# Optimization experiments

Measured on AMD Instinct MI355X. Metric: run time of the kernel, lower is better.

Reference implementation:

```python
import jax, jax.numpy as jnp
import numpy as np

N, D_IN, D_H, D_OUT, E = 32768, 1024, 2048, 1024, 8

def setup_inputs() -> dict:
    key = jax.random.key(0)
    ks = jax.random.split(key, 8)
    s_in = 1.0 / np.sqrt(D_IN)
    s_h = 1.0 / np.sqrt(D_H)
    return {
        "x": jax.random.normal(ks[0], (N, D_IN), dtype=jnp.float32),
        "Wr": jax.random.normal(ks[1], (D_IN, E), dtype=jnp.float32) * s_in,
        "br": jnp.zeros((E,), dtype=jnp.float32),
        "W1": jax.random.normal(ks[2], (E, D_IN, D_H), dtype=jnp.float32) * s_in,
        "b1": jnp.zeros((E, D_H), dtype=jnp.float32),
        "W2": jax.random.normal(ks[3], (E, D_H, D_OUT), dtype=jnp.float32) * s_h,
        "b2": jnp.zeros((E, D_OUT), dtype=jnp.float32),
    }

def reference(x, Wr, br, W1, b1, W2, b2):
    # Supervised router: encoder is Identity, router is Linear + softmax.
    router_probs = jax.nn.softmax(x @ Wr + br, axis=-1)            # [N, E]
    router_probs_max = jnp.max(router_probs, axis=-1)              # [N]
    routes = jnp.argmax(router_probs, axis=-1)                     # [N] int
    counts = jnp.sum(jax.nn.one_hot(routes, E, dtype=x.dtype), axis=0)  # [E]

    # Top-1 dispatch: each token goes through exactly one expert MLP.
    # Small fixed loop over experts (E=8); mask-combine replaces gather/scatter.
    out = jnp.zeros((N, D_OUT), dtype=x.dtype)
    for e in range(E):
        h = jax.nn.relu(x @ W1[e] + b1[e])                         # [N, D_H]
        y = h @ W2[e] + b2[e]                                      # [N, D_OUT]
        out = out + jnp.where((routes == e)[:, None], y, jnp.zeros((), x.dtype))
    # Straight-through scaling: value 1 in fwd, routes grad through router prob.
    scale = router_probs_max / jax.lax.stop_gradient(router_probs_max)
    out = out * scale[:, None]
    return out, router_probs, counts
```

## Files before the change

### kernel.cpp

```cpp
#include <hip/hip_runtime.h>
#include <stdint.h>


#define NTOK   32768
#define DIN    1024
#define DH     2048
#define DOUT   1024
#define NEXP   8

typedef unsigned short u16;
typedef __bf16 bf16x8 __attribute__((ext_vector_type(8)));
typedef float  f32x4  __attribute__((ext_vector_type(4)));
typedef const __attribute__((address_space(1))) void gvoid_t;
typedef __attribute__((address_space(3))) void svoid_t;

__device__ __forceinline__ u16 f2bf(float f) {
  union { float f; uint32_t u; } v; v.f = f;
  return (u16)((v.u + 0x7FFFu + ((v.u >> 16) & 1u)) >> 16);
}

__global__ __launch_bounds__(256) void k_router(
    const float* __restrict__ x, const float* __restrict__ Wr,
    const float* __restrict__ br, float* __restrict__ probs,
    int* __restrict__ routes, u16* __restrict__ xb)
{
  __shared__ float wr_s[NEXP * DIN];
  int tid = threadIdx.x;
  for (int idx = tid; idx < DIN * NEXP / 4; idx += 256) {
    float4 v = ((const float4*)Wr)[idx];
    int k = idx >> 1, r = (idx & 1) * 4;
    wr_s[(r + 0) * DIN + k] = v.x;
    wr_s[(r + 1) * DIN + k] = v.y;
    wr_s[(r + 2) * DIN + k] = v.z;
    wr_s[(r + 3) * DIN + k] = v.w;
  }
  __syncthreads();
  int lane = tid & 63, wv = tid >> 6;
  int t = blockIdx.x * 4 + wv;
  const float* xr = x + (size_t)t * DIN;
  u16* xbrow = xb + (size_t)t * DIN;
  float acc[NEXP];
  #pragma unroll
  for (int e = 0; e < NEXP; ++e) acc[e] = 0.f;
  #pragma unroll
  for (int i = 0; i < 4; ++i) {
    int k = i * 256 + lane * 4;
    float4 xv = *(const float4*)(xr + k);
    ushort4 o;
    o.x = f2bf(xv.x); o.y = f2bf(xv.y); o.z = f2bf(xv.z); o.w = f2bf(xv.w);
    *(ushort4*)(xbrow + k) = o;
    #pragma unroll
    for (int e = 0; e < NEXP; ++e) {
      float4 w4 = *(const float4*)(wr_s + e * DIN + k);
      acc[e] += xv.x * w4.x + xv.y * w4.y + xv.z * w4.z + xv.w * w4.w;
    }
  }
  #pragma unroll
  for (int off = 32; off >= 1; off >>= 1) {
    #pragma unroll
    for (int e = 0; e < NEXP; ++e) acc[e] += __shfl_xor(acc[e], off, 64);
  }
  if (lane == 0) {
    float l[NEXP], m = -1e30f;
    #pragma unroll
    for (int e = 0; e < NEXP; ++e) { l[e] = acc[e] + br[e]; m = fmaxf(m, l[e]); }
    float p[NEXP], s = 0.f;
    #pragma unroll
    for (int e = 0; e < NEXP; ++e) { p[e] = expf(l[e] - m); s += p[e]; }
    float inv = 1.f / s;
    int am = 0; float best = l[0];
    #pragma unroll
    for (int e = 1; e < NEXP; ++e) if (l[e] > best) { best = l[e]; am = e; }
    #pragma unroll
    for (int e = 0; e < NEXP; ++e) probs[(size_t)t * NEXP + e] = p[e] * inv;
    routes[t] = am;
  }
}

__global__ __launch_bounds__(256) void k_count(
    const int* __restrict__ routes, int* __restrict__ aux)
{
  int t = blockIdx.x * 256 + threadIdx.x;
  int e = routes[t];
  int lane = threadIdx.x & 63;
  #pragma unroll
  for (int ee = 0; ee < NEXP; ++ee) {
    unsigned long long m = __ballot(e == ee);
    if (lane == 0 && m) atomicAdd(&aux[ee], (int)__popcll(m));
  }
}

__global__ __launch_bounds__(256) void k_prefix(int* __restrict__ aux, float* __restrict__ counts_out)
{
  __shared__ int s_off[NEXP], s_cnt[NEXP], s_tb[NEXP], s_nt;
  int tid = threadIdx.x;
  if (tid == 0) {
    int off = 0, tb = 0;
    for (int e = 0; e < NEXP; ++e) {
      int c = aux[e];
      counts_out[e] = (float)c;
      s_cnt[e] = c; s_off[e] = off; s_tb[e] = tb;
      aux[24 + e] = off;
      off += c; tb += (c + 127) >> 7;
    }
    s_nt = tb;
    aux[16] = tb;
  }
  __syncthreads();
  int nt = s_nt;
  for (int i = tid; i < nt; i += 256) {
    int e = 0;
    #pragma unroll
    for (int k = 1; k < NEXP; ++k) if (i >= s_tb[k]) e = k;
    int tt = i - s_tb[e];
    aux[128 + i] = e;
    aux[512 + i] = s_off[e] + tt * 128;
    aux[896 + i] = s_off[e] + s_cnt[e];
  }
}

__global__ __launch_bounds__(256) void k_assign(
    const int* __restrict__ routes, int* __restrict__ aux,
    int* __restrict__ pos_of_tok, int* __restrict__ tok_of_pos)
{
  int t = blockIdx.x * 256 + threadIdx.x;
  int e = routes[t];
  int lane = threadIdx.x & 63;
  int p = 0;
  #pragma unroll
  for (int ee = 0; ee < NEXP; ++ee) {
    unsigned long long m = __ballot(e == ee);
    int base = 0;
    if (lane == 0 && m) base = atomicAdd(&aux[8 + ee], (int)__popcll(m));
    base = __shfl(base, 0, 64);
    if (e == ee)
      p = aux[24 + ee] + base + (int)__popcll(m & ((1ull << lane) - 1ull));
  }
  pos_of_tok[t] = p;
  tok_of_pos[p] = t;
}

__global__ __launch_bounds__(256) void k_transpose(
    const float* __restrict__ W1, u16* __restrict__ W1t,
    const float* __restrict__ W2, u16* __restrict__ W2t)
{
  int z = blockIdx.z;
  const float* src; u16* dst; int K, Nn, e;
  if (z < NEXP) { src = W1; dst = W1t; K = DIN; Nn = DH;   e = z; }
  else          { src = W2; dst = W2t; K = DH;  Nn = DOUT; e = z - NEXP; }
  int k0 = blockIdx.x * 64, n0 = blockIdx.y * 64;
  if (k0 >= K || n0 >= Nn) return;
  __shared__ float tile[64][65];
  const float* s = src + ((size_t)e * K + k0) * Nn + n0;
  int r = threadIdx.x >> 6, c = threadIdx.x & 63;
  #pragma unroll
  for (int i = 0; i < 16; ++i)
    tile[r + i * 4][c] = s[(size_t)(r + i * 4) * Nn + c];
  __syncthreads();
  u16* d = dst + ((size_t)e * Nn + n0) * K + k0;
  #pragma unroll
  for (int i = 0; i < 16; ++i) {
    int nr = r + i * 4;
    d[(size_t)nr * K + c] = f2bf(tile[c][nr]);
  }
}

template<int MODE, int GATHER>
__global__ __launch_bounds__(256, 4) void k_gemm(
    const u16* __restrict__ A, const u16* __restrict__ Bt,
    const float* __restrict__ bias, u16* __restrict__ Hout,
    float* __restrict__ Yout, const int* __restrict__ tok_of_pos,
    const int* __restrict__ aux, int K, int Nn, int nbyl)
{
  int nwg = gridDim.x;
  int bid = blockIdx.x;
  int wg  = (bid & 7) * (nwg >> 3) + (bid >> 3);
  int by  = wg & ((1 << nbyl) - 1);
  int bx  = wg >> nbyl;
  if (bx >= aux[16]) return;
  int e  = aux[128 + bx];
  int r0 = aux[512 + bx];
  int r1 = aux[896 + bx];
  int bn0 = by << 7;

  __shared__ __align__(16) u16 As[128 * 64];
  __shared__ __align__(16) u16 Bs[128 * 64];

  int tid = threadIdx.x;
  int lane = tid & 63, wv = tid >> 6;
  int wr = wv >> 1, wc = wv & 1;
  const u16* Be = Bt + (size_t)e * Nn * K;

  int tk[4];
  #pragma unroll
  for (int r = 0; r < 4; ++r) {
    int gr = r0 + r * 32 + (tid >> 3);
    gr = gr < NTOK ? gr : NTOK - 1;
    tk[r] = GATHER ? tok_of_pos[gr] : gr;
  }

  auto stage = [&](int kt) {
    int k0 = kt * 64;
    #pragma unroll
    for (int r = 0; r < 4; ++r) {
      int L = (r * 256 + tid) * 16;
      int sl = ((L >> 4) & 7) ^ ((L >> 7) & 7);
      __builtin_amdgcn_global_load_lds(
          (gvoid_t*)((const char*)(A + (size_t)tk[r] * K + k0) + sl * 16),
          (svoid_t*)((char*)As + L), 16, 0, 0);
    }
    #pragma unroll
    for (int r = 0; r < 4; ++r) {
      int L = (r * 256 + tid) * 16;
      int row = L >> 7;
      int sl = ((L >> 4) & 7) ^ (row & 7);
      __builtin_amdgcn_global_load_lds(
          (gvoid_t*)((const char*)(Be + (size_t)(bn0 + row) * K + k0) + sl * 16),
          (svoid_t*)((char*)Bs + L), 16, 0, 0);
    }
  };

  f32x4 acc[4][4];
  #pragma unroll
  for (int i = 0; i < 4; ++i)
    #pragma unroll
    for (int j = 0; j < 4; ++j)
      acc[i][j] = (f32x4){0.f, 0.f, 0.f, 0.f};

  int KT = K >> 6;
  stage(0);
  for (int kt = 0; kt < KT; ++kt) {
    __syncthreads();
    const char* As_c = (const char*)As;
    const char* Bs_c = (const char*)Bs;
    #pragma unroll
    for (int kk = 0; kk < 2; ++kk) {
      int sw = ((kk * 4 + (lane >> 4)) ^ (lane & 7)) << 4;
      bf16x8 a[4], b[4];
      #pragma unroll
      for (int f = 0; f < 4; ++f)
        a[f] = *(const bf16x8*)(As_c + (wr * 64 + f * 16 + (lane & 15)) * 128 + sw);
      #pragma unroll
      for (int f = 0; f < 4; ++f)
        b[f] = *(const bf16x8*)(Bs_c + (wc * 64 + f * 16 + (lane & 15)) * 128 + sw);
      #pragma unroll
      for (int i = 0; i < 4; ++i)
        #pragma unroll
        for (int j = 0; j < 4; ++j)
          acc[i][j] = __builtin_amdgcn_mfma_f32_16x16x32_bf16(a[i], b[j], acc[i][j], 0, 0, 0);
    }
    __syncthreads();
    if (kt + 1 < KT) stage(kt + 1);
  }

  const float* be = bias + (size_t)e * Nn;
  float bv[4];
  #pragma unroll
  for (int j = 0; j < 4; ++j) bv[j] = be[bn0 + wc * 64 + j * 16 + (lane & 15)];
  #pragma unroll
  for (int i = 0; i < 4; ++i) {
    #pragma unroll
    for (int q = 0; q < 4; ++q) {
      int r = r0 + wr * 64 + i * 16 + (lane >> 4) * 4 + q;
      if (r < r1) {
        if (MODE == 0) {
          u16* dst = Hout + (size_t)r * Nn + bn0 + wc * 64 + (lane & 15);
          #pragma unroll
          for (int j = 0; j < 4; ++j)
            dst[j * 16] = f2bf(fmaxf(acc[i][j][q] + bv[j], 0.f));
        } else {
          int tok = tok_of_pos[r];
          float* dst = Yout + (size_t)tok * Nn + bn0 + wc * 64 + (lane & 15);
          #pragma unroll
          for (int j = 0; j < 4; ++j)
            dst[j * 16] = acc[i][j][q] + bv[j];
        }
      }
    }
  }
}

extern "C" void kernel_launch(void* const* d_in, const int* in_sizes, int n_in,
                              void* d_out, int out_size, void* d_ws, size_t ws_size,
                              hipStream_t stream)
{
  const float* x  = (const float*)d_in[0];
  const float* Wr = (const float*)d_in[1];
  const float* br = (const float*)d_in[2];
  const float* W1 = (const float*)d_in[3];
  const float* b1 = (const float*)d_in[4];
  const float* W2 = (const float*)d_in[5];
  const float* b2 = (const float*)d_in[6];

  float* out    = (float*)d_out;
  float* probs  = out + (size_t)NTOK * DOUT;
  float* counts = probs + (size_t)NTOK * NEXP;

  char* ws = (char*)d_ws;
  u16* xb          = (u16*)(ws);
  u16* h           = (u16*)(ws + 67108864);
  u16* W1t         = (u16*)(ws + 201326592);
  u16* W2t         = (u16*)(ws + 234881024);
  int* aux         = (int*)(ws + 268435456);
  int* routes      = (int*)(ws + 268451840);
  int* pos_of_tok  = (int*)(ws + 268582912);
  int* tok_of_pos  = (int*)(ws + 268713984);

  (void)hipMemsetAsync(aux, 0, 16384, stream);
  k_router<<<NTOK / 4, 256, 0, stream>>>(x, Wr, br, probs, routes, xb);
  k_count<<<NTOK / 256, 256, 0, stream>>>(routes, aux);
  k_transpose<<<dim3(32, 32, 2 * NEXP), 256, 0, stream>>>(W1, W1t, W2, W2t);
  k_prefix<<<1, 256, 0, stream>>>(aux, counts);
  k_assign<<<NTOK / 256, 256, 0, stream>>>(routes, aux, pos_of_tok, tok_of_pos);
  k_gemm<0, 1><<<264 * 16, 256, 0, stream>>>(xb, W1t, b1, h, nullptr, tok_of_pos, aux, DIN, DH, 4);
  k_gemm<1, 0><<<264 * 8, 256, 0, stream>>>(h, W2t, b2, nullptr, out, tok_of_pos, aux, DH, DOUT, 3);
}
```

Baseline: 526.2 us.

## Switch expert GEMMs to 256x256 tiles with 8 waves and double-buffered LDS pipeline

Rewrites the grouped expert GEMM to use 512-thread workgroups computing 256x256 output tiles, with double-buffered LDS stages and hand-scheduled phases. Each phase interleaves global-to-LDS prefetch with MFMA bursts, using explicit barriers, waitcnt and setprio. Row-tile size in the prefix kernel moves to 256 to match, and the router writes probabilities as two float4 stores. The goal is more data reuse per tile and latency hiding of loads, at the cost of more padding waste per expert and lower occupancy. The 0-padded grid counts (135*8, 136*4) must cover the new tile counts.

```diff
diff --git a/kernel.cpp b/kernel.cpp
--- a/kernel.cpp
+++ b/kernel.cpp
@@ -71,8 +71,10 @@
     int am = 0; float best = l[0];
     #pragma unroll
     for (int e = 1; e < NEXP; ++e) if (l[e] > best) { best = l[e]; am = e; }
-    #pragma unroll
-    for (int e = 0; e < NEXP; ++e) probs[(size_t)t * NEXP + e] = p[e] * inv;
+    float4 pa = {p[0] * inv, p[1] * inv, p[2] * inv, p[3] * inv};
+    float4 pb = {p[4] * inv, p[5] * inv, p[6] * inv, p[7] * inv};
+    float4* pd = (float4*)(probs + (size_t)t * NEXP);
+    pd[0] = pa; pd[1] = pb;
     routes[t] = am;
   }
 }
@@ -101,7 +103,7 @@
       counts_out[e] = (float)c;
       s_cnt[e] = c; s_off[e] = off; s_tb[e] = tb;
       aux[24 + e] = off;
-      off += c; tb += (c + 127) >> 7;
+      off += c; tb += (c + 255) >> 8;
     }
     s_nt = tb;
     aux[16] = tb;
@@ -114,7 +116,7 @@
     for (int k = 1; k < NEXP; ++k) if (i >= s_tb[k]) e = k;
     int tt = i - s_tb[e];
     aux[128 + i] = e;
-    aux[512 + i] = s_off[e] + tt * 128;
+    aux[512 + i] = s_off[e] + tt * 256;
     aux[896 + i] = s_off[e] + s_cnt[e];
   }
 }
@@ -165,8 +167,31 @@
   }
 }
 
+
+#define FENCE() __builtin_amdgcn_sched_barrier(0)
+#define BARX()  do { FENCE(); __builtin_amdgcn_s_barrier(); FENCE(); } while (0)
+#define LGKM0() do { asm volatile("s_waitcnt lgkmcnt(0)" ::: "memory"); FENCE(); } while (0)
+#define VMC6()  do { asm volatile("s_waitcnt vmcnt(6)" ::: "memory"); FENCE(); } while (0)
+
+#define PH_TAIL(I0, J0)                                                              \
+  do {                                                                               \
+    BARX(); LGKM0();                                                                 \
+    __builtin_amdgcn_s_setprio(1);                                                   \
+    _Pragma("unroll")                                                                \
+    for (int ii = 0; ii < 4; ++ii)                                                   \
+      _Pragma("unroll")                                                              \
+      for (int jj = 0; jj < 2; ++jj) {                                               \
+        acc[(I0)+ii][(J0)+jj] = __builtin_amdgcn_mfma_f32_16x16x32_bf16(             \
+            aF[ii][0], bF[(J0)+jj][0], acc[(I0)+ii][(J0)+jj], 0, 0, 0);              \
+        acc[(I0)+ii][(J0)+jj] = __builtin_amdgcn_mfma_f32_16x16x32_bf16(             \
+            aF[ii][1], bF[(J0)+jj][1], acc[(I0)+ii][(J0)+jj], 0, 0, 0);              \
+      }                                                                              \
+    __builtin_amdgcn_s_setprio(0);                                                   \
+    BARX();                                                                          \
+  } while (0)
+
 template<int MODE, int GATHER>
-__global__ __launch_bounds__(256, 4) void k_gemm(
+__global__ __launch_bounds__(512, 2) void k_gemm8(
     const u16* __restrict__ A, const u16* __restrict__ Bt,
     const float* __restrict__ bias, u16* __restrict__ Hout,
     float* __restrict__ Yout, const int* __restrict__ tok_of_pos,
@@ -181,87 +206,134 @@
   int e  = aux[128 + bx];
   int r0 = aux[512 + bx];
   int r1 = aux[896 + bx];
-  int bn0 = by << 7;
-
-  __shared__ __align__(16) u16 As[128 * 64];
-  __shared__ __align__(16) u16 Bs[128 * 64];
+  int bn0 = by << 8;
+
+  __shared__ __align__(16) u16 lds[2][2][16384];
 
   int tid = threadIdx.x;
   int lane = tid & 63, wv = tid >> 6;
-  int wr = wv >> 1, wc = wv & 1;
-  const u16* Be = Bt + (size_t)e * Nn * K;
-
-  int tk[4];
-  #pragma unroll
-  for (int r = 0; r < 4; ++r) {
-    int gr = r0 + r * 32 + (tid >> 3);
-    gr = gr < NTOK ? gr : NTOK - 1;
-    tk[r] = GATHER ? tok_of_pos[gr] : gr;
-  }
-
-  auto stage = [&](int kt) {
-    int k0 = kt * 64;
-    #pragma unroll
-    for (int r = 0; r < 4; ++r) {
-      int L = (r * 256 + tid) * 16;
-      int sl = ((L >> 4) & 7) ^ ((L >> 7) & 7);
-      __builtin_amdgcn_global_load_lds(
-          (gvoid_t*)((const char*)(A + (size_t)tk[r] * K + k0) + sl * 16),
-          (svoid_t*)((char*)As + L), 16, 0, 0);
-    }
-    #pragma unroll
-    for (int r = 0; r < 4; ++r) {
-      int L = (r * 256 + tid) * 16;
-      int row = L >> 7;
-      int sl = ((L >> 4) & 7) ^ (row & 7);
-      __builtin_amdgcn_global_load_lds(
-          (gvoid_t*)((const char*)(Be + (size_t)(bn0 + row) * K + k0) + sl * 16),
-          (svoid_t*)((char*)Bs + L), 16, 0, 0);
+  int wr = wv >> 2, wc = wv & 3;
+  const u16* Be = Bt + (size_t)e * (size_t)Nn * K;
+
+  int tkA[4];
+  #pragma unroll
+  for (int c = 0; c < 4; ++c) {
+    int row = (c >> 1) * 128 + (c & 1) * 64 + (tid >> 3);
+    int gr = r0 + row; gr = gr < NTOK ? gr : NTOK - 1;
+    tkA[c] = GATHER ? tok_of_pos[gr] : gr;
+  }
+
+  char* ldsA0 = (char*)&lds[0][0][0]; char* ldsA1 = (char*)&lds[1][0][0];
+  char* ldsB0 = (char*)&lds[0][1][0]; char* ldsB1 = (char*)&lds[1][1][0];
+
+  auto stageA = [&](char* base, int kt, int h) {
+    int k0 = kt << 6;
+    #pragma unroll
+    for (int r = 0; r < 2; ++r) {
+      int off = (r * 512 + tid) * 16;
+      int sl = ((off >> 4) & 7) ^ ((off >> 7) & 7);
+      const char* src = (const char*)(A + (size_t)tkA[h * 2 + r] * K + k0) + sl * 16;
+      __builtin_amdgcn_global_load_lds((gvoid_t*)src,
+          (svoid_t*)(base + h * 16384 + off), 16, 0, 0);
     }
   };
-
-  f32x4 acc[4][4];
-  #pragma unroll
-  for (int i = 0; i < 4; ++i)
+  auto stageB = [&](char* base, int kt, int h) {
+    int k0 = kt << 6;
+    #pragma unroll
+    for (int r = 0; r < 2; ++r) {
+      int off = (r * 512 + tid) * 16;
+      int row = h * 128 + (off >> 7);
+      int sl = ((off >> 4) & 7) ^ (row & 7);
+      const char* src = (const char*)(Be + (size_t)(bn0 + row) * K + k0) + sl * 16;
+      __builtin_amdgcn_global_load_lds((gvoid_t*)src,
+          (svoid_t*)(base + h * 16384 + off), 16, 0, 0);
+    }
+  };
+  auto lda = [&](const char* base, int i, int kk) -> bf16x8 {
+    int row = wr * 128 + i * 16 + (lane & 15);
+    int sw = ((kk * 4 + (lane >> 4)) ^ (lane & 7)) << 4;
+    return *(const bf16x8*)(base + row * 128 + sw);
+  };
+  auto ldb = [&](const char* base, int j, int kk) -> bf16x8 {
+    int row = wc * 64 + j * 16 + (lane & 15);
+    int sw = ((kk * 4 + (lane >> 4)) ^ (lane & 7)) << 4;
+    return *(const bf16x8*)(base + row * 128 + sw);
+  };
+
+  f32x4 acc[8][4];
+  #pragma unroll
+  for (int i = 0; i < 8; ++i)
     #pragma unroll
     for (int j = 0; j < 4; ++j)
       acc[i][j] = (f32x4){0.f, 0.f, 0.f, 0.f};
 
-  int KT = K >> 6;
-  stage(0);
-  for (int kt = 0; kt < KT; ++kt) {
-    __syncthreads();
-    const char* As_c = (const char*)As;
-    const char* Bs_c = (const char*)Bs;
-    #pragma unroll
-    for (int kk = 0; kk < 2; ++kk) {
-      int sw = ((kk * 4 + (lane >> 4)) ^ (lane & 7)) << 4;
-      bf16x8 a[4], b[4];
-      #pragma unroll
-      for (int f = 0; f < 4; ++f)
-        a[f] = *(const bf16x8*)(As_c + (wr * 64 + f * 16 + (lane & 15)) * 128 + sw);
-      #pragma unroll
-      for (int f = 0; f < 4; ++f)
-        b[f] = *(const bf16x8*)(Bs_c + (wc * 64 + f * 16 + (lane & 15)) * 128 + sw);
-      #pragma unroll
-      for (int i = 0; i < 4; ++i)
-        #pragma unroll
-        for (int j = 0; j < 4; ++j)
-          acc[i][j] = __builtin_amdgcn_mfma_f32_16x16x32_bf16(a[i], b[j], acc[i][j], 0, 0, 0);
-    }
-    __syncthreads();
-    if (kt + 1 < KT) stage(kt + 1);
-  }
+  int KT = K >> 6, NI = KT >> 1;
+
+  stageA(ldsA0, 0, 0); stageA(ldsA0, 0, 1);
+  stageB(ldsB0, 0, 0); stageB(ldsB0, 0, 1);
+  stageB(ldsB1, 1, 0); stageB(ldsB1, 1, 1);
+  stageA(ldsA1, 1, 0);
+  VMC6(); BARX();
+
+  for (int it = 0; it < NI; ++it) {
+    int t1 = 2 * it + 1;
+    int s2 = 2 * it + 2; if (s2 >= KT) s2 = KT - 2;
+    int s3 = 2 * it + 3; if (s3 >= KT) s3 = KT - 1;
+    bf16x8 aF[4][2], bF[4][2];
+
+    #pragma unroll
+    for (int ii = 0; ii < 4; ++ii) { aF[ii][0] = lda(ldsA0, ii, 0); aF[ii][1] = lda(ldsA0, ii, 1); }
+    #pragma unroll
+    for (int jj = 0; jj < 2; ++jj) { bF[jj][0] = ldb(ldsB0, jj, 0); bF[jj][1] = ldb(ldsB0, jj, 1); }
+    stageA(ldsA1, t1, 1);
+    PH_TAIL(0, 0);
+
+    #pragma unroll
+    for (int jj = 2; jj < 4; ++jj) { bF[jj][0] = ldb(ldsB0, jj, 0); bF[jj][1] = ldb(ldsB0, jj, 1); }
+    PH_TAIL(0, 2);
+
+    #pragma unroll
+    for (int ii = 0; ii < 4; ++ii) { aF[ii][0] = lda(ldsA0, 4 + ii, 0); aF[ii][1] = lda(ldsA0, 4 + ii, 1); }
+    stageB(ldsB0, s2, 0);
+    PH_TAIL(4, 0);
+
+    stageB(ldsB0, s2, 1);
+    stageA(ldsA0, s2, 0);
+    VMC6();
+    PH_TAIL(4, 2);
+
+    #pragma unroll
+    for (int ii = 0; ii < 4; ++ii) { aF[ii][0] = lda(ldsA1, ii, 0); aF[ii][1] = lda(ldsA1, ii, 1); }
+    #pragma unroll
+    for (int jj = 0; jj < 2; ++jj) { bF[jj][0] = ldb(ldsB1, jj, 0); bF[jj][1] = ldb(ldsB1, jj, 1); }
+    stageA(ldsA0, s2, 1);
+    PH_TAIL(0, 0);
+
+    #pragma unroll
+    for (int jj = 2; jj < 4; ++jj) { bF[jj][0] = ldb(ldsB1, jj, 0); bF[jj][1] = ldb(ldsB1, jj, 1); }
+    PH_TAIL(0, 2);
+
+    #pragma unroll
+    for (int ii = 0; ii < 4; ++ii) { aF[ii][0] = lda(ldsA1, 4 + ii, 0); aF[ii][1] = lda(ldsA1, 4 + ii, 1); }
+    stageB(ldsB1, s3, 0);
+    PH_TAIL(4, 0);
+
+    stageB(ldsB1, s3, 1);
+    stageA(ldsA1, s3, 0);
+    VMC6();
+    PH_TAIL(4, 2);
+  }
+  asm volatile("s_waitcnt vmcnt(0)" ::: "memory");
 
   const float* be = bias + (size_t)e * Nn;
   float bv[4];
   #pragma unroll
   for (int j = 0; j < 4; ++j) bv[j] = be[bn0 + wc * 64 + j * 16 + (lane & 15)];
   #pragma unroll
-  for (int i = 0; i < 4; ++i) {
+  for (int i = 0; i < 8; ++i) {
     #pragma unroll
     for (int q = 0; q < 4; ++q) {
-      int r = r0 + wr * 64 + i * 16 + (lane >> 4) * 4 + q;
+      int r = r0 + wr * 128 + i * 16 + (lane >> 4) * 4 + q;
       if (r < r1) {
         if (MODE == 0) {
           u16* dst = Hout + (size_t)r * Nn + bn0 + wc * 64 + (lane & 15);
@@ -312,6 +384,6 @@
   k_transpose<<<dim3(32, 32, 2 * NEXP), 256, 0, stream>>>(W1, W1t, W2, W2t);
   k_prefix<<<1, 256, 0, stream>>>(aux, counts);
   k_assign<<<NTOK / 256, 256, 0, stream>>>(routes, aux, pos_of_tok, tok_of_pos);
-  k_gemm<0, 1><<<264 * 16, 256, 0, stream>>>(xb, W1t, b1, h, nullptr, tok_of_pos, aux, DIN, DH, 4);
-  k_gemm<1, 0><<<264 * 8, 256, 0, stream>>>(h, W2t, b2, nullptr, out, tok_of_pos, aux, DH, DOUT, 3);
-}
+  k_gemm8<0, 1><<<135 * 8, 512, 0, stream>>>(xb, W1t, b1, h, nullptr, tok_of_pos, aux, DIN, DH, 3);
+  k_gemm8<1, 0><<<136 * 4, 512, 0, stream>>>(h, W2t, b2, nullptr, out, tok_of_pos, aux, DH, DOUT, 2);
+}
```

After: 554.4 us. 1.05x slower.
